# Kernel tuning notes

Measured on AMD Instinct MI355X. Metric: run time of the kernel, lower is better.

Reference implementation:

```python
import jax, jax.numpy as jnp
import numpy as np

DIM = 1024
HEADS = 16
HDIM = DIM // HEADS
MLP_HID = 4096
LN_EPS = 1e-5
NORM_EPS = 1e-12  # F.normalize eps


def _layernorm(x, g, b):
    mu = jnp.mean(x, axis=-1, keepdims=True)
    var = jnp.mean(jnp.square(x - mu), axis=-1, keepdims=True)
    return (x - mu) / jnp.sqrt(var + LN_EPS) * g + b


def _l2norm(x):
    n = jnp.linalg.norm(x, axis=-1, keepdims=True)
    return x / jnp.maximum(n, NORM_EPS)


def setup_inputs() -> dict:
    key = jax.random.key(0)
    ks = jax.random.split(key, 8)
    s = 0.02
    x = jax.random.normal(ks[0], (2, 2048, DIM), dtype=jnp.float32)
    w_qkv = jax.random.normal(ks[1], (3 * DIM, DIM), dtype=jnp.float32) * s  # torch Linear weight (out,in)
    w_proj = jax.random.normal(ks[2], (DIM, DIM), dtype=jnp.float32) * s
    temp = jnp.ones((HEADS, 1, 1), dtype=jnp.float32)
    w1 = jax.random.normal(ks[3], (MLP_HID, DIM), dtype=jnp.float32) * s
    b1 = jnp.zeros((MLP_HID,), dtype=jnp.float32)
    w2 = jax.random.normal(ks[4], (DIM, MLP_HID), dtype=jnp.float32) * s
    b2 = jnp.zeros((DIM,), dtype=jnp.float32)
    ln1_g = jnp.ones((DIM,), dtype=jnp.float32)
    ln1_b = jnp.zeros((DIM,), dtype=jnp.float32)
    ln2_g = jnp.ones((DIM,), dtype=jnp.float32)
    ln2_b = jnp.zeros((DIM,), dtype=jnp.float32)
    return {"x": x, "ln1_g": ln1_g, "ln1_b": ln1_b, "w_qkv": w_qkv,
            "w_proj": w_proj, "temp": temp, "ln2_g": ln2_g, "ln2_b": ln2_b,
            "w1": w1, "b1": b1, "w2": w2, "b2": b2}


def reference(x, ln1_g, ln1_b, w_qkv, w_proj, temp, ln2_g, ln2_b, w1, b1, w2, b2):
    b, n, c = x.shape
    # --- MHSA with L2-normalized q,k and learnable per-head temperature ---
    h = _layernorm(x, ln1_g, ln1_b)
    qkv = h @ w_qkv.T                             # [b,n,3c]
    qkv = qkv.reshape(b, n, 3, HEADS, HDIM).transpose(2, 0, 3, 1, 4)  # [3,b,h,n,d]
    q, k, v = qkv[0], qkv[1], qkv[2]
    q = _l2norm(q)
    k = _l2norm(k)
    attn = jnp.einsum('bhnd,bhmd->bhnm', q, k) * temp  # temp [h,1,1] broadcasts
    attn = jax.nn.softmax(attn, axis=-1)
    out = jnp.einsum('bhnm,bhmd->bhnd', attn, v)       # [b,h,n,d]
    out = out.transpose(0, 2, 1, 3).reshape(b, n, c)
    x = x + out @ w_proj.T
    # --- MLP ---
    h = _layernorm(x, ln2_g, ln2_b)
    h = jax.nn.gelu(h @ w1.T + b1, approximate=False)
    x = x + h @ w2.T + b2
    return x
```

## Files before the change

### kernel.cpp

```cpp
#include <hip/hip_runtime.h>
#include <cstdint>
#include <cstddef>

typedef unsigned short u16;
typedef __attribute__((ext_vector_type(8))) short short8;
typedef __attribute__((ext_vector_type(4))) float f32x4;
typedef __attribute__((ext_vector_type(4))) float float4v;
typedef __attribute__((ext_vector_type(4))) u16 u16x4;

__device__ __forceinline__ u16 f2bf(float f) {
  union { float f; uint32_t u; } v; v.f = f;
  uint32_t u = v.u;
  return (u16)((u + 0x7FFFu + ((u >> 16) & 1u)) >> 16);
}
__device__ __forceinline__ float bf2f(u16 s) {
  union { uint32_t u; float f; } v; v.u = ((uint32_t)s) << 16; return v.f;
}

__device__ __forceinline__ float fast_exp2(float x) {
#if __has_builtin(__builtin_amdgcn_exp2f)
  return __builtin_amdgcn_exp2f(x);
#else
  return exp2f(x);
#endif
}

__device__ __forceinline__ void gload16(const u16* g, u16* l) {
  __builtin_amdgcn_global_load_lds((const __attribute__((address_space(1))) void*)g,
                                   (__attribute__((address_space(3))) void*)l,
                                   16, 0, 0);
}

__global__ __launch_bounds__(256) void k_cvt(const float* __restrict__ in, u16* __restrict__ out, int n4) {
  int i = blockIdx.x * 256 + threadIdx.x;
  if (i >= n4) return;
  float4v v = *(const float4v*)(in + (size_t)i * 4);
  u16x4 o;
  #pragma unroll
  for (int j = 0; j < 4; j++) o[j] = f2bf(v[j]);
  *(u16x4*)(out + (size_t)i * 4) = o;
}

__global__ __launch_bounds__(256) void k_ln(const float* __restrict__ x, const float* __restrict__ g,
                                            const float* __restrict__ b, u16* __restrict__ out) {
  int row = blockIdx.x, tid = threadIdx.x;
  int wid = tid >> 6;
  const float* xr = x + (size_t)row * 1024;
  float4v v = *(const float4v*)(xr + tid * 4);
  float s = v[0] + v[1] + v[2] + v[3];
  float sq = v[0]*v[0] + v[1]*v[1] + v[2]*v[2] + v[3]*v[3];
  #pragma unroll
  for (int m = 1; m <= 32; m <<= 1) { s += __shfl_xor(s, m); sq += __shfl_xor(sq, m); }
  __shared__ float ss[4], ssq[4];
  if ((tid & 63) == 0) { ss[wid] = s; ssq[wid] = sq; }
  __syncthreads();
  s = ss[0] + ss[1] + ss[2] + ss[3];
  sq = ssq[0] + ssq[1] + ssq[2] + ssq[3];
  float mu = s * (1.0f/1024.0f);
  float var = sq * (1.0f/1024.0f) - mu*mu;
  float rs = rsqrtf(var + 1e-5f);
  u16x4 o;
  #pragma unroll
  for (int j = 0; j < 4; j++) {
    float y = (v[j] - mu) * rs * g[tid*4+j] + b[tid*4+j];
    o[j] = f2bf(y);
  }
  *(u16x4*)(out + (size_t)row * 1024 + tid * 4) = o;
}

template<int EPI>
__global__ __launch_bounds__(512, 2) void k_g256(const u16* __restrict__ A, const u16* __restrict__ B,
                                                 const float* __restrict__ bias, u16* __restrict__ Cb,
                                                 int M, int N, int K, int Ksub) {
  extern __shared__ __align__(16) u16 smem[];
  int tid = threadIdx.x;
  int gx = gridDim.x;
  int lin = blockIdx.y * gx + blockIdx.x;
  int nwg = gx * gridDim.y;
  int cpx = nwg >> 3;
  int swz = (lin & 7) * cpx + (lin >> 3);
  int bx = swz % gx, by = swz / gx;
  int m0 = by * 256, n0 = bx * 256;
  int kbase = blockIdx.z * Ksub;
  int wid = tid >> 6, lane = tid & 63;
  int wm = wid >> 2, wn = wid & 3;
  int l15 = lane & 15, l16 = lane >> 4;

  f32x4 acc[8][4] = {};
  int nt = Ksub >> 5;

  auto STAGE = [&](int bsel, int kb) {
    u16* abase = smem + bsel * 16384;
    u16* bbase = abase + 8192;
    #pragma unroll
    for (int i = 0; i < 2; i++) {
      int c = i*512 + tid;
      int R = c >> 3, p = c & 7;
      int sp = p ^ (R & 7);
      int r = 2*R + (sp >> 2);
      int g = sp & 3;
      gload16(A + (size_t)(m0 + r)*K + kb + g*8, abase + c*8);
      gload16(B + (size_t)(n0 + r)*K + kb + g*8, bbase + c*8);
    }
  };

  STAGE(0, kbase);
  STAGE(1, kbase + 32);

  for (int t = 0; t < nt; ++t) {
    if (t + 1 < nt) asm volatile("s_waitcnt vmcnt(4)" ::: "memory");
    else            asm volatile("s_waitcnt vmcnt(0)" ::: "memory");
    __builtin_amdgcn_sched_barrier(0);
    __builtin_amdgcn_s_barrier();
    __builtin_amdgcn_sched_barrier(0);
    if (t + 2 < nt) STAGE((t + 2) % 3, kbase + (t + 2) * 32);
    const u16* ab = smem + (t % 3) * 16384;
    const u16* bb = ab + 8192;
    short8 af[8], bf[4];
    #pragma unroll
    for (int mf = 0; mf < 8; mf++) {
      int r = wm*128 + mf*16 + l15;
      int R = r >> 1;
      int sp = ((r & 1)*4 + l16) ^ (R & 7);
      af[mf] = *(const short8*)(ab + R*64 + sp*8);
    }
    #pragma unroll
    for (int nf = 0; nf < 4; nf++) {
      int r = wn*64 + nf*16 + l15;
      int R = r >> 1;
      int sp = ((r & 1)*4 + l16) ^ (R & 7);
      bf[nf] = *(const short8*)(bb + R*64 + sp*8);
    }
    asm volatile("s_waitcnt lgkmcnt(0)" ::: "memory");
    __builtin_amdgcn_sched_barrier(0);
    __builtin_amdgcn_s_setprio(1);
    #pragma unroll
    for (int mf = 0; mf < 8; mf++)
      #pragma unroll
      for (int nf = 0; nf < 4; nf++)
        acc[mf][nf] = __builtin_amdgcn_mfma_f32_16x16x32_bf16(af[mf], bf[nf], acc[mf][nf], 0, 0, 0);
    __builtin_amdgcn_s_setprio(0);
  }

  size_t zoff = (EPI == 6) ? (size_t)blockIdx.z * M * N : 0;
  #pragma unroll
  for (int mf = 0; mf < 8; mf++) {
    #pragma unroll
    for (int nf = 0; nf < 4; nf++) {
      int col = n0 + wn*64 + nf*16 + l15;
      #pragma unroll
      for (int r = 0; r < 4; r++) {
        int row = m0 + wm*128 + mf*16 + l16*4 + r;
        float v = acc[mf][nf][r];
        if constexpr (EPI == 2) { v += bias[col]; v = 0.5f*v*(1.0f + erff(v*0.70710678118f)); }
        Cb[zoff + (size_t)row*N + col] = f2bf(v);
      }
    }
  }
}

template<int HASB>
__global__ __launch_bounds__(256) void k_red4(const float* __restrict__ base, const float* __restrict__ bias,
                                              const u16* __restrict__ P, float* __restrict__ out) {
  int i = blockIdx.x * 256 + threadIdx.x;
  float4v v = *(const float4v*)(base + (size_t)i * 4);
  if constexpr (HASB) {
    float4v bb = *(const float4v*)(bias + (size_t)(i & 255) * 4);
    #pragma unroll
    for (int j = 0; j < 4; j++) v[j] += bb[j];
  }
  #pragma unroll
  for (int z = 0; z < 4; z++) {
    u16x4 p = *(const u16x4*)(P + (size_t)z * 4194304 + (size_t)i * 4);
    #pragma unroll
    for (int j = 0; j < 4; j++) v[j] += bf2f(p[j]);
  }
  *(float4v*)(out + (size_t)i * 4) = v;
}

__global__ __launch_bounds__(256) void k_prep(const u16* __restrict__ qkv, const float* __restrict__ temp,
                                              u16* __restrict__ Qn, u16* __restrict__ Kn, u16* __restrict__ Vt) {
  int grp = blockIdx.x, bh = blockIdx.y;
  int b = bh >> 4, h = bh & 15;
  int tid = threadIdx.x, wid = tid >> 6, lane = tid & 63;
  int n0 = grp * 64;
  __shared__ __align__(16) u16 vs[64*64];
  float tmp = temp[h] * 1.44269504f;
  for (int j = 0; j < 16; j++) {
    int tl = wid + 4*j;
    size_t roff = (size_t)((b*2048) + n0 + tl) * 3072;
    float q = bf2f(qkv[roff + h*64 + lane]);
    float k = bf2f(qkv[roff + 1024 + h*64 + lane]);
    u16 vraw = qkv[roff + 2048 + h*64 + lane];
    float sq = q*q, sk = k*k;
    #pragma unroll
    for (int m = 1; m <= 32; m <<= 1) { sq += __shfl_xor(sq, m); sk += __shfl_xor(sk, m); }
    float qs = tmp / fmaxf(sqrtf(sq), 1e-12f);
    float ksc = 1.0f / fmaxf(sqrtf(sk), 1e-12f);
    size_t obase = ((size_t)bh*2048 + n0 + tl)*64 + lane;
    Qn[obase] = f2bf(q * qs);
    Kn[obase] = f2bf(k * ksc);
    vs[tl*64 + lane] = vraw;
  }
  __syncthreads();
  int d = tid & 63, chunk = tid >> 6;
  u16 vals[16];
  #pragma unroll
  for (int jj = 0; jj < 16; jj++) vals[jj] = vs[(chunk*16 + jj)*64 + d];
  short8 w0, w1v;
  #pragma unroll
  for (int j = 0; j < 8; j++) { w0[j] = (short)vals[j]; w1v[j] = (short)vals[8+j]; }
  size_t vo = ((size_t)bh*64 + d)*2048 + n0 + chunk*16;
  *(short8*)(Vt + vo) = w0;
  *(short8*)(Vt + vo + 8) = w1v;
}

__global__ __launch_bounds__(256) void k_attn(const u16* __restrict__ Qn, const u16* __restrict__ Kn,
                                              const u16* __restrict__ Vt, const float* __restrict__ temp,
                                              u16* __restrict__ Out) {
  __shared__ __align__(16) u16 Ks[2][64*64];
  __shared__ __align__(16) u16 Vs[2][64*64];
  __shared__ __align__(16) u16 Ps[4*16*64];
  int qg = blockIdx.x, bh = blockIdx.y;
  int b = bh >> 4, h = bh & 15;
  int tid = threadIdx.x, wid = tid >> 6, lane = tid & 63;
  int l15 = lane & 15, l16 = lane >> 4;
  size_t base = (size_t)bh * 2048 * 64;
  size_t vbase = (size_t)bh * 64 * 2048;
  int q0 = qg*64 + wid*16;
  float m2 = fabsf(temp[h]) * 1.44269504f;
  short8 qf[2];
  #pragma unroll
  for (int ks = 0; ks < 2; ks++)
    qf[ks] = *(const short8*)(Qn + base + (size_t)(q0 + l15)*64 + ks*32 + l16*8);
  f32x4 o[4] = {};
  float lrow = 0.f;
  u16* Pw = Ps + wid*16*64;
  uint32_t* Pw32 = (uint32_t*)Pw;

  auto STAGE = [&](int bsel, int kv0) {
    #pragma unroll
    for (int i = 0; i < 2; i++) {
      int base_row = wid*16 + i*8;
      int row = base_row + (lane >> 3);
      int gslot = (lane & 7) ^ (row & 7);
      gload16(Kn + base + (size_t)(kv0 + row)*64 + gslot*8, &Ks[bsel][base_row*64]);
      gload16(Vt + vbase + (size_t)row*2048 + kv0 + gslot*8, &Vs[bsel][base_row*64]);
    }
  };

  STAGE(0, 0);
  __syncthreads();
  int cur = 0;
  for (int kv0 = 0; kv0 < 2048; kv0 += 64) {
    if (kv0 + 64 < 2048) STAGE(cur ^ 1, kv0 + 64);
    f32x4 s[4] = {};
    #pragma unroll
    for (int ks = 0; ks < 2; ks++) {
      short8 kf[4];
      #pragma unroll
      for (int nt = 0; nt < 4; nt++) {
        int row = nt*16 + l15;
        kf[nt] = *(const short8*)&Ks[cur][row*64 + (((ks*4 + l16) ^ (row&7))*8)];
      }
      #pragma unroll
      for (int nt = 0; nt < 4; nt++)
        s[nt] = __builtin_amdgcn_mfma_f32_16x16x32_bf16(kf[nt], qf[ks], s[nt], 0, 0, 0);
    }
    float tsum = 0.f;
    #pragma unroll
    for (int nt = 0; nt < 4; nt++) {
      #pragma unroll
      for (int rp = 0; rp < 2; rp++) {
        float p0 = fast_exp2(s[nt][2*rp]   - m2);
        float p1 = fast_exp2(s[nt][2*rp+1] - m2);
        tsum += p0 + p1;
        uint32_t pk;
        asm("v_cvt_pk_bf16_f32 %0, %1, %2" : "=v"(pk) : "v"(p0), "v"(p1));
        int w = nt*8 + l16*2 + rp;
        int slot = w >> 2;
        Pw32[l15*32 + ((slot ^ (l15 & 7))*4) + (w & 3)] = pk;
      }
    }
    lrow += tsum;
    asm volatile("s_waitcnt lgkmcnt(0)" ::: "memory");
    __builtin_amdgcn_sched_barrier(0);
    #pragma unroll
    for (int ks = 0; ks < 2; ks++) {
      short8 pf = *(const short8*)&Pw[l15*64 + (((ks*4 + l16) ^ (l15&7))*8)];
      short8 vf[4];
      #pragma unroll
      for (int dt = 0; dt < 4; dt++) {
        int row = dt*16 + l15;
        vf[dt] = *(const short8*)&Vs[cur][row*64 + (((ks*4 + l16) ^ (row&7))*8)];
      }
      #pragma unroll
      for (int dt = 0; dt < 4; dt++)
        o[dt] = __builtin_amdgcn_mfma_f32_16x16x32_bf16(vf[dt], pf, o[dt], 0, 0, 0);
    }
    __syncthreads();
    cur ^= 1;
  }
  lrow += __shfl_xor(lrow, 16);
  lrow += __shfl_xor(lrow, 32);
  float rl = 1.0f / lrow;
  int tok = b*2048 + q0 + l15;
  #pragma unroll
  for (int dt = 0; dt < 4; dt++) {
    u16x4 ov;
    #pragma unroll
    for (int r = 0; r < 4; r++) ov[r] = f2bf(o[dt][r] * rl);
    *(u16x4*)(Out + (size_t)tok*1024 + h*64 + dt*16 + l16*4) = ov;
  }
}

static constexpr size_t OFF_WQKV  = 0;
static constexpr size_t OFF_WPROJ = OFF_WQKV  + 6291456;
static constexpr size_t OFF_W1    = OFF_WPROJ + 2097152;
static constexpr size_t OFF_W2    = OFF_W1    + 8388608;
static constexpr size_t OFF_HBF   = OFF_W2    + 8388608;
static constexpr size_t OFF_H2BF  = OFF_HBF   + 8388608;
static constexpr size_t OFF_QKVBF = OFF_H2BF  + 8388608;
static constexpr size_t OFF_QN    = OFF_QKVBF + 25165824;
static constexpr size_t OFF_KN    = OFF_QN    + 8388608;
static constexpr size_t OFF_VT    = OFF_KN    + 8388608;
static constexpr size_t OFF_AOUT  = OFF_VT    + 8388608;
static constexpr size_t OFF_X1    = OFF_AOUT  + 8388608;
static constexpr size_t OFF_HID   = OFF_X1    + 16777216;

extern "C" void kernel_launch(void* const* d_in, const int* in_sizes, int n_in,
                              void* d_out, int out_size, void* d_ws, size_t ws_size,
                              hipStream_t stream) {
  (void)in_sizes; (void)n_in; (void)out_size; (void)ws_size;
  const float* x     = (const float*)d_in[0];
  const float* ln1g  = (const float*)d_in[1];
  const float* ln1b  = (const float*)d_in[2];
  const float* wqkv  = (const float*)d_in[3];
  const float* wproj = (const float*)d_in[4];
  const float* temp  = (const float*)d_in[5];
  const float* ln2g  = (const float*)d_in[6];
  const float* ln2b  = (const float*)d_in[7];
  const float* w1    = (const float*)d_in[8];
  const float* b1    = (const float*)d_in[9];
  const float* w2    = (const float*)d_in[10];
  const float* b2    = (const float*)d_in[11];

  char* ws = (char*)d_ws;
  u16* wqkv_bf  = (u16*)(ws + OFF_WQKV);
  u16* wproj_bf = (u16*)(ws + OFF_WPROJ);
  u16* w1_bf    = (u16*)(ws + OFF_W1);
  u16* w2_bf    = (u16*)(ws + OFF_W2);
  u16* h_bf     = (u16*)(ws + OFF_HBF);
  u16* h2_bf    = (u16*)(ws + OFF_H2BF);
  u16* qkv_bf   = (u16*)(ws + OFF_QKVBF);
  u16* Qn       = (u16*)(ws + OFF_QN);
  u16* Kn       = (u16*)(ws + OFF_KN);
  u16* Vt       = (u16*)(ws + OFF_VT);
  u16* aout_bf  = (u16*)(ws + OFF_AOUT);
  float* x1     = (float*)(ws + OFF_X1);
  u16* hid_bf   = (u16*)(ws + OFF_HID);
  u16* part_p   = (u16*)(ws + OFF_HID);
  u16* part_m   = (u16*)(ws + OFF_QN);
  float* outf   = (float*)d_out;

  static bool attr_done = false;
  if (!attr_done) {
    hipFuncSetAttribute((const void*)k_g256<2>, hipFuncAttributeMaxDynamicSharedMemorySize, 98304);
    hipFuncSetAttribute((const void*)k_g256<4>, hipFuncAttributeMaxDynamicSharedMemorySize, 98304);
    hipFuncSetAttribute((const void*)k_g256<6>, hipFuncAttributeMaxDynamicSharedMemorySize, 98304);
    attr_done = true;
  }

  k_cvt<<<3072, 256, 0, stream>>>(wqkv,  wqkv_bf,  786432);
  k_cvt<<<1024, 256, 0, stream>>>(wproj, wproj_bf, 262144);
  k_cvt<<<4096, 256, 0, stream>>>(w1,    w1_bf,    1048576);
  k_cvt<<<4096, 256, 0, stream>>>(w2,    w2_bf,    1048576);

  k_ln<<<4096, 256, 0, stream>>>(x, ln1g, ln1b, h_bf);
  k_g256<4><<<dim3(12, 16), 512, 98304, stream>>>(h_bf, wqkv_bf, nullptr, qkv_bf, 4096, 3072, 1024, 1024);
  k_prep<<<dim3(32, 32), 256, 0, stream>>>(qkv_bf, temp, Qn, Kn, Vt);
  k_attn<<<dim3(32, 32), 256, 0, stream>>>(Qn, Kn, Vt, temp, aout_bf);
  k_g256<6><<<dim3(4, 16, 4), 512, 98304, stream>>>(aout_bf, wproj_bf, nullptr, part_p, 4096, 1024, 1024, 256);
  k_red4<0><<<4096, 256, 0, stream>>>(x, nullptr, part_p, x1);
  k_ln<<<4096, 256, 0, stream>>>(x1, ln2g, ln2b, h2_bf);
  k_g256<2><<<dim3(16, 16), 512, 98304, stream>>>(h2_bf, w1_bf, b1, hid_bf, 4096, 4096, 1024, 1024);
  k_g256<6><<<dim3(4, 16, 4), 512, 98304, stream>>>(hid_bf, w2_bf, nullptr, part_m, 4096, 1024, 4096, 1024);
  k_red4<1><<<4096, 256, 0, stream>>>(x1, b2, part_m, outf);
}
```

Measured before the change: 268.5 us.

## Double attention query tile per wave, fuse proj reduction with LayerNorm, remap attn grid

The attention kernel now gives each wave 32 query rows instead of 16, so every K/V tile loaded into shared memory feeds twice as many MFMAs. The grid is halved and block indices are remapped so that neighbouring blocks share the same batch-head. This is meant to cut K/V traffic and LDS reads per unit of work, at the cost of more registers and a larger P buffer in shared memory. Separately, the projection split-K reduction and LayerNorm2 are fused into one kernel, which removes a launch and a round trip of x1 through memory.

```diff
diff --git a/kernel.cpp b/kernel.cpp
--- a/kernel.cpp
+++ b/kernel.cpp
@@ -66,6 +66,38 @@
     o[j] = f2bf(y);
   }
   *(u16x4*)(out + (size_t)row * 1024 + tid * 4) = o;
+}
+
+__global__ __launch_bounds__(256) void k_redln(const float* __restrict__ x, const u16* __restrict__ P,
+                                               const float* __restrict__ g, const float* __restrict__ b,
+                                               float* __restrict__ x1, u16* __restrict__ h2) {
+  int row = blockIdx.x, tid = threadIdx.x;
+  int wid = tid >> 6;
+  size_t off = (size_t)row * 1024 + tid * 4;
+  float4v v = *(const float4v*)(x + off);
+  #pragma unroll
+  for (int z = 0; z < 4; z++) {
+    u16x4 p = *(const u16x4*)(P + (size_t)z * 4194304 + off);
+    #pragma unroll
+    for (int j = 0; j < 4; j++) v[j] += bf2f(p[j]);
+  }
+  *(float4v*)(x1 + off) = v;
+  float s = v[0] + v[1] + v[2] + v[3];
+  float sq = v[0]*v[0] + v[1]*v[1] + v[2]*v[2] + v[3]*v[3];
+  #pragma unroll
+  for (int m = 1; m <= 32; m <<= 1) { s += __shfl_xor(s, m); sq += __shfl_xor(sq, m); }
+  __shared__ float ss[4], ssq[4];
+  if ((tid & 63) == 0) { ss[wid] = s; ssq[wid] = sq; }
+  __syncthreads();
+  s = ss[0] + ss[1] + ss[2] + ss[3];
+  sq = ssq[0] + ssq[1] + ssq[2] + ssq[3];
+  float mu = s * (1.0f/1024.0f);
+  float var = sq * (1.0f/1024.0f) - mu*mu;
+  float rs = rsqrtf(var + 1e-5f);
+  u16x4 o;
+  #pragma unroll
+  for (int j = 0; j < 4; j++) o[j] = f2bf((v[j] - mu) * rs * g[tid*4+j] + b[tid*4+j]);
+  *(u16x4*)(h2 + off) = o;
 }
 
 template<int EPI>
@@ -220,22 +252,27 @@
                                               u16* __restrict__ Out) {
   __shared__ __align__(16) u16 Ks[2][64*64];
   __shared__ __align__(16) u16 Vs[2][64*64];
-  __shared__ __align__(16) u16 Ps[4*16*64];
-  int qg = blockIdx.x, bh = blockIdx.y;
+  __shared__ __align__(16) u16 Ps[4*2*16*64];
+  int lin = blockIdx.y * gridDim.x + blockIdx.x;
+  int c = lin & 7, t5 = lin >> 3;
+  int bh = c*4 + (t5 >> 4);
+  int qg = t5 & 15;
   int b = bh >> 4, h = bh & 15;
   int tid = threadIdx.x, wid = tid >> 6, lane = tid & 63;
   int l15 = lane & 15, l16 = lane >> 4;
   size_t base = (size_t)bh * 2048 * 64;
   size_t vbase = (size_t)bh * 64 * 2048;
-  int q0 = qg*64 + wid*16;
+  int q0 = qg*128 + wid*32;
   float m2 = fabsf(temp[h]) * 1.44269504f;
-  short8 qf[2];
-  #pragma unroll
-  for (int ks = 0; ks < 2; ks++)
-    qf[ks] = *(const short8*)(Qn + base + (size_t)(q0 + l15)*64 + ks*32 + l16*8);
-  f32x4 o[4] = {};
-  float lrow = 0.f;
-  u16* Pw = Ps + wid*16*64;
+  short8 qf[2][2];
+  #pragma unroll
+  for (int g = 0; g < 2; g++)
+    #pragma unroll
+    for (int ks = 0; ks < 2; ks++)
+      qf[g][ks] = *(const short8*)(Qn + base + (size_t)(q0 + g*16 + l15)*64 + ks*32 + l16*8);
+  f32x4 o[2][4] = {};
+  float lrow[2] = {0.f, 0.f};
+  u16* Pw = Ps + wid*2048;
   uint32_t* Pw32 = (uint32_t*)Pw;
 
   auto STAGE = [&](int bsel, int kv0) {
@@ -254,7 +291,7 @@
   int cur = 0;
   for (int kv0 = 0; kv0 < 2048; kv0 += 64) {
     if (kv0 + 64 < 2048) STAGE(cur ^ 1, kv0 + 64);
-    f32x4 s[4] = {};
+    f32x4 s[2][4] = {};
     #pragma unroll
     for (int ks = 0; ks < 2; ks++) {
       short8 kf[4];
@@ -264,53 +301,65 @@
         kf[nt] = *(const short8*)&Ks[cur][row*64 + (((ks*4 + l16) ^ (row&7))*8)];
       }
       #pragma unroll
-      for (int nt = 0; nt < 4; nt++)
-        s[nt] = __builtin_amdgcn_mfma_f32_16x16x32_bf16(kf[nt], qf[ks], s[nt], 0, 0, 0);
-    }
-    float tsum = 0.f;
-    #pragma unroll
-    for (int nt = 0; nt < 4; nt++) {
-      #pragma unroll
-      for (int rp = 0; rp < 2; rp++) {
-        float p0 = fast_exp2(s[nt][2*rp]   - m2);
-        float p1 = fast_exp2(s[nt][2*rp+1] - m2);
-        tsum += p0 + p1;
-        uint32_t pk;
-        asm("v_cvt_pk_bf16_f32 %0, %1, %2" : "=v"(pk) : "v"(p0), "v"(p1));
-        int w = nt*8 + l16*2 + rp;
-        int slot = w >> 2;
-        Pw32[l15*32 + ((slot ^ (l15 & 7))*4) + (w & 3)] = pk;
-      }
-    }
-    lrow += tsum;
+      for (int nt = 0; nt < 4; nt++) {
+        s[0][nt] = __builtin_amdgcn_mfma_f32_16x16x32_bf16(kf[nt], qf[0][ks], s[0][nt], 0, 0, 0);
+        s[1][nt] = __builtin_amdgcn_mfma_f32_16x16x32_bf16(kf[nt], qf[1][ks], s[1][nt], 0, 0, 0);
+      }
+    }
+    #pragma unroll
+    for (int g = 0; g < 2; g++) {
+      float tsum = 0.f;
+      #pragma unroll
+      for (int nt = 0; nt < 4; nt++) {
+        #pragma unroll
+        for (int rp = 0; rp < 2; rp++) {
+          float p0 = fast_exp2(s[g][nt][2*rp]   - m2);
+          float p1 = fast_exp2(s[g][nt][2*rp+1] - m2);
+          tsum += p0 + p1;
+          uint32_t pk;
+          asm("v_cvt_pk_bf16_f32 %0, %1, %2" : "=v"(pk) : "v"(p0), "v"(p1));
+          int w = nt*8 + l16*2 + rp;
+          int slot = w >> 2;
+          Pw32[g*512 + l15*32 + ((slot ^ (l15 & 7))*4) + (w & 3)] = pk;
+        }
+      }
+      lrow[g] += tsum;
+    }
     asm volatile("s_waitcnt lgkmcnt(0)" ::: "memory");
     __builtin_amdgcn_sched_barrier(0);
     #pragma unroll
     for (int ks = 0; ks < 2; ks++) {
-      short8 pf = *(const short8*)&Pw[l15*64 + (((ks*4 + l16) ^ (l15&7))*8)];
       short8 vf[4];
       #pragma unroll
       for (int dt = 0; dt < 4; dt++) {
         int row = dt*16 + l15;
         vf[dt] = *(const short8*)&Vs[cur][row*64 + (((ks*4 + l16) ^ (row&7))*8)];
       }
-      #pragma unroll
-      for (int dt = 0; dt < 4; dt++)
-        o[dt] = __builtin_amdgcn_mfma_f32_16x16x32_bf16(vf[dt], pf, o[dt], 0, 0, 0);
+      short8 pf0 = *(const short8*)&Pw[0*1024 + l15*64 + (((ks*4 + l16) ^ (l15&7))*8)];
+      short8 pf1 = *(const short8*)&Pw[1*1024 + l15*64 + (((ks*4 + l16) ^ (l15&7))*8)];
+      #pragma unroll
+      for (int dt = 0; dt < 4; dt++) {
+        o[0][dt] = __builtin_amdgcn_mfma_f32_16x16x32_bf16(vf[dt], pf0, o[0][dt], 0, 0, 0);
+        o[1][dt] = __builtin_amdgcn_mfma_f32_16x16x32_bf16(vf[dt], pf1, o[1][dt], 0, 0, 0);
+      }
     }
     __syncthreads();
     cur ^= 1;
   }
-  lrow += __shfl_xor(lrow, 16);
-  lrow += __shfl_xor(lrow, 32);
-  float rl = 1.0f / lrow;
-  int tok = b*2048 + q0 + l15;
-  #pragma unroll
-  for (int dt = 0; dt < 4; dt++) {
-    u16x4 ov;
-    #pragma unroll
-    for (int r = 0; r < 4; r++) ov[r] = f2bf(o[dt][r] * rl);
-    *(u16x4*)(Out + (size_t)tok*1024 + h*64 + dt*16 + l16*4) = ov;
+  #pragma unroll
+  for (int g = 0; g < 2; g++) {
+    float l = lrow[g];
+    l += __shfl_xor(l, 16);
+    l += __shfl_xor(l, 32);
+    float rl = 1.0f / l;
+    int tok = b*2048 + q0 + g*16 + l15;
+    #pragma unroll
+    for (int dt = 0; dt < 4; dt++) {
+      u16x4 ov;
+      #pragma unroll
+      for (int r = 0; r < 4; r++) ov[r] = f2bf(o[g][dt][r] * rl);
+      *(u16x4*)(Out + (size_t)tok*1024 + h*64 + dt*16 + l16*4) = ov;
+    }
   }
 }
 
@@ -379,10 +428,9 @@
   k_ln<<<4096, 256, 0, stream>>>(x, ln1g, ln1b, h_bf);
   k_g256<4><<<dim3(12, 16), 512, 98304, stream>>>(h_bf, wqkv_bf, nullptr, qkv_bf, 4096, 3072, 1024, 1024);
   k_prep<<<dim3(32, 32), 256, 0, stream>>>(qkv_bf, temp, Qn, Kn, Vt);
-  k_attn<<<dim3(32, 32), 256, 0, stream>>>(Qn, Kn, Vt, temp, aout_bf);
+  k_attn<<<dim3(16, 32), 256, 0, stream>>>(Qn, Kn, Vt, temp, aout_bf);
   k_g256<6><<<dim3(4, 16, 4), 512, 98304, stream>>>(aout_bf, wproj_bf, nullptr, part_p, 4096, 1024, 1024, 256);
-  k_red4<0><<<4096, 256, 0, stream>>>(x, nullptr, part_p, x1);
-  k_ln<<<4096, 256, 0, stream>>>(x1, ln2g, ln2b, h2_bf);
+  k_redln<<<4096, 256, 0, stream>>>(x, part_p, ln2g, ln2b, x1, h2_bf);
   k_g256<2><<<dim3(16, 16), 512, 98304, stream>>>(h2_bf, w1_bf, b1, hid_bf, 4096, 4096, 1024, 1024);
   k_g256<6><<<dim3(4, 16, 4), 512, 98304, stream>>>(hid_bf, w2_bf, nullptr, part_m, 4096, 1024, 4096, 1024);
   k_red4<1><<<4096, 256, 0, stream>>>(x1, b2, part_m, outf);
```

Result: faster. 260.8 us (-2.9%).
